# Optimization experiments

Measured on AMD Instinct MI355X. Metric: run time of the kernel, lower is better.

The kernel has to match this reference:

```python
import jax, jax.numpy as jnp
import numpy as np

# static config matching init_kwargs
NODE, K, KER, STR = 32, 10, 5, 2
B, C = 8, 64
N = NODE * NODE          # 1024 nodes per sample
BN = B * N               # 8192 total nodes
OUT = (NODE - KER) // STR + 1
E = OUT * OUT            # local hyperedges per sample (196)
BN_EPS = 1e-5


def _local_block_diag():
    """Static block-diagonal local incidence matrix (BN, B*E), built once in numpy."""
    idx = np.arange(N).reshape(NODE, NODE)
    H_local = np.zeros((N, E), np.float32)
    e = 0
    for i in range(0, NODE - KER + 1, STR):
        for j in range(0, NODE - KER + 1, STR):
            H_local[idx[i:i + KER, j:j + KER].ravel(), e] = 1.0
            e += 1
    blk = np.zeros((BN, B * E), np.float32)
    for b in range(B):
        blk[b * N:(b + 1) * N, b * E:(b + 1) * E] = H_local
    return jnp.asarray(blk)


_LOCAL_BLK = _local_block_diag()


def setup_inputs() -> dict:
    key = jax.random.key(0)
    k1, k2 = jax.random.split(key, 2)
    x = jax.random.normal(k1, (B, N, C), jnp.float32)
    W_conv = jax.random.normal(k2, (C, C), jnp.float32) * 0.05
    b_conv = jnp.zeros((C,), jnp.float32)
    gamma = jnp.ones((C,), jnp.float32)
    beta = jnp.zeros((C,), jnp.float32)
    return {"x": x, "W_conv": W_conv, "b_conv": b_conv, "gamma": gamma, "beta": beta}


def reference(x, W_conv, b_conv, gamma, beta):
    xm = x.reshape(BN, C)                       # merged nodes (B*N, C)

    # --- hypergraph construction (no_grad in torch) ---
    xs = jax.lax.stop_gradient(xm)
    sq = jnp.sum(xs * xs, axis=-1, keepdims=True)
    dists = sq - 2.0 * (xs @ xs.T) + sq.T       # (BN, BN) pairwise sq-dists
    _, inds = jax.lax.top_k(-dists, K + 1)      # K+1 smallest distances
    # weights_function(prob=False) -> all ones; scatter incidence
    H = jnp.zeros((BN, BN), x.dtype).at[jnp.arange(BN)[:, None], inds].set(1.0)
    # Dv == K+1 for every row -> max_k = K+1 and the second topk gives new_H == H
    Hfull = jnp.concatenate([H, _LOCAL_BLK], axis=1)  # (BN, BN + B*E)

    # G = Dv^{-1/2} H W De^{-1} H^T Dv^{-1/2}, W = I, via diagonal scaling
    DV = Hfull.sum(axis=1)
    DE = jnp.maximum(Hfull.sum(axis=0), 1e-8)
    dv2 = DV ** -0.5
    A = dv2[:, None] * Hfull
    G = (A * (1.0 / DE)[None, :]) @ A.T          # (BN, BN)
    G = jax.lax.stop_gradient(G)

    # --- HGNN conv: linear -> G matmul -> BN (train stats) -> relu -> residual ---
    y = xm @ W_conv.T + b_conv                   # (BN, C)
    z = G @ y                                    # (BN, C)
    mu = z.mean(axis=0)
    var = z.var(axis=0)                          # biased, as torch BN training
    zn = (z - mu) / jnp.sqrt(var + BN_EPS) * gamma + beta
    out = jax.nn.relu(zn) + xm
    return out.reshape(B, N, C)
```

## Files before the change

kernel.cpp:

```cpp
#include <hip/hip_runtime.h>
#include <math.h>

#define BNTOT 8192
#define CH    64
#define KP1   11
#define NLOC  1568
#define MARGIN 1.0f
#define LCAPR 256

typedef __attribute__((ext_vector_type(8))) short short8;
typedef __attribute__((ext_vector_type(4))) float float4v;

__device__ __forceinline__ int pcnt(int p) {
  int lo = p - 4; if (lo < 0) lo = 0; lo += (lo & 1);
  int hi = p; if (hi > 26) hi = 26;
  return (hi >= lo) ? (((hi - lo) >> 1) + 1) : 0;
}
__device__ __forceinline__ float dv2_of(int u) {
  int node = u & 1023;
  int rr = node >> 5, cc = node & 31;
  int dv = KP1 + pcnt(rr) * pcnt(cc);
  return 1.0f / sqrtf((float)dv);
}
__device__ __forceinline__ unsigned short f2bf(float f) {
  unsigned u = __float_as_uint(f);
  unsigned r = (u + 0x7FFFu + ((u >> 16) & 1u)) >> 16;
  return (unsigned short)r;
}
__device__ __forceinline__ unsigned fkey(float s) {
  unsigned u = __float_as_uint(s);
  return (u & 0x80000000u) ? ~u : (u | 0x80000000u);
}
__device__ __forceinline__ unsigned long long skey(float s, int idx) {
  return ((unsigned long long)fkey(s) << 32) | (unsigned)idx;
}
__device__ __forceinline__ int mbcnt64(unsigned long long m) {
  return __builtin_amdgcn_mbcnt_hi((unsigned)(m >> 32),
         __builtin_amdgcn_mbcnt_lo((unsigned)m, 0));
}

__global__ void k_cast(const float* __restrict__ X, unsigned short* __restrict__ Xh,
                       float* __restrict__ sq) {
  int g = blockIdx.x * 256 + threadIdx.x;
  int lane = threadIdx.x & 63;
  float v = X[g];
  Xh[g] = f2bf(v);
  float s = v * v;
  #pragma unroll
  for (int off = 32; off >= 1; off >>= 1) s += __shfl_xor(s, off, 64);
  if (lane == 0) sq[g >> 6] = s;
}

__global__ __launch_bounds__(256)
void k_thrpart(const float* __restrict__ X, const float* __restrict__ sq,
               float* __restrict__ part) {
  const int tid = threadIdx.x, wave = tid >> 6, lane = tid & 63;
  const int rg = blockIdx.x >> 3, chunk = blockIdx.x & 7;
  const int row = rg * 64 + lane;
  float xr[CH];
  {
    const float4* xp = (const float4*)(X + (size_t)row * CH);
    #pragma unroll
    for (int k = 0; k < CH / 4; ++k) {
      float4 v = xp[k];
      xr[4*k+0] = v.x; xr[4*k+1] = v.y; xr[4*k+2] = v.z; xr[4*k+3] = v.w;
    }
  }
  float tv[KP1];
  #pragma unroll
  for (int t = 0; t < KP1; ++t) tv[t] = INFINITY;

  for (int s = 0; s < 32; ++s) {
    int j = __builtin_amdgcn_readfirstlane(((chunk * 4 + wave) * 32 + s) * 8);
    const float* cp = X + (size_t)j * CH;
    float d0 = 0.f, d1 = 0.f, d2 = 0.f, d3 = 0.f;
    #pragma unroll
    for (int k = 0; k < CH / 4; ++k) {
      d0 = fmaf(xr[4*k+0], cp[4*k+0], d0);
      d1 = fmaf(xr[4*k+1], cp[4*k+1], d1);
      d2 = fmaf(xr[4*k+2], cp[4*k+2], d2);
      d3 = fmaf(xr[4*k+3], cp[4*k+3], d3);
    }
    float cv = fmaf(-2.0f, (d0 + d1) + (d2 + d3), sq[j]);
    #pragma unroll
    for (int t = 0; t < KP1; ++t) {
      float lo = fminf(tv[t], cv), hi = fmaxf(tv[t], cv);
      tv[t] = lo; cv = hi;
    }
  }
  __shared__ float ls[4][64][KP1];
  #pragma unroll
  for (int t = 0; t < KP1; ++t) ls[wave][lane][t] = tv[t];
  __syncthreads();
  if (tid < 64) {
    float v[KP1];
    #pragma unroll
    for (int t = 0; t < KP1; ++t) v[t] = ls[0][tid][t];
    #pragma unroll
    for (int w = 1; w < 4; ++w)
      #pragma unroll
      for (int t = 0; t < KP1; ++t) {
        float cv = ls[w][tid][t];
        #pragma unroll
        for (int s2 = 0; s2 < KP1; ++s2) {
          float lo = fminf(v[s2], cv), hi = fmaxf(v[s2], cv);
          v[s2] = lo; cv = hi;
        }
      }
    size_t base = ((size_t)blockIdx.x * 64 + tid) * KP1;
    #pragma unroll
    for (int t = 0; t < KP1; ++t) part[base + t] = v[t];
  }
}

__global__ void k_thrmerge(const float* __restrict__ part, float* __restrict__ thr) {
  const int rg = blockIdx.x, lane = threadIdx.x;
  const int row = rg * 64 + lane;
  float v[KP1];
  {
    size_t b0 = ((size_t)(rg * 8) * 64 + lane) * KP1;
    #pragma unroll
    for (int t = 0; t < KP1; ++t) v[t] = part[b0 + t];
  }
  for (int c = 1; c < 8; ++c) {
    size_t b = ((size_t)(rg * 8 + c) * 64 + lane) * KP1;
    #pragma unroll
    for (int t = 0; t < KP1; ++t) {
      float cv = part[b + t];
      #pragma unroll
      for (int s2 = 0; s2 < KP1; ++s2) {
        float lo = fminf(v[s2], cv), hi = fmaxf(v[s2], cv);
        v[s2] = lo; cv = hi;
      }
    }
  }
  thr[row] = v[KP1 - 1] + MARGIN;
}

__global__ __launch_bounds__(256)
void k_filter(const unsigned short* __restrict__ Xh, const float* __restrict__ sq,
              const float* __restrict__ thr, unsigned long long* __restrict__ mask) {
  const int tid = threadIdx.x, wave = tid >> 6, lane = tid & 63;
  const int m = lane & 15, q = lane >> 4;
  const int rowbase = (blockIdx.x >> 5) * 64;
  const int colbase = (blockIdx.x & 31) * 256 + wave * 64;
  const int wcol = (blockIdx.x & 31) * 4 + wave;

  short8 a[4][2];
  #pragma unroll
  for (int rt = 0; rt < 4; ++rt)
    #pragma unroll
    for (int kc = 0; kc < 2; ++kc)
      a[rt][kc] = *(const short8*)(Xh + (size_t)(rowbase + rt * 16 + m) * CH + kc * 32 + q * 8);

  short8 b0[4], b1[4];
  float sqv[4];
  #pragma unroll
  for (int sub = 0; sub < 4; ++sub) {
    const int coln = colbase + sub * 16 + m;
    const short8* bp = (const short8*)(Xh + (size_t)coln * CH + q * 8);
    b0[sub] = bp[0];
    b1[sub] = bp[4];
    sqv[sub] = sq[coln];
  }

  float thrv[16];
  #pragma unroll
  for (int rt = 0; rt < 4; ++rt)
    #pragma unroll
    for (int r = 0; r < 4; ++r)
      thrv[rt * 4 + r] = thr[rowbase + rt * 16 + q * 4 + r];

  const float4v cz = {0.f, 0.f, 0.f, 0.f};
  const int sr = lane & 15, qq = sr >> 2, rr = sr & 3;

  #pragma unroll
  for (int rt = 0; rt < 4; ++rt) {
    unsigned long long bal[4][4];
    #pragma unroll
    for (int sub = 0; sub < 4; ++sub) {
      float4v c = __builtin_amdgcn_mfma_f32_16x16x32_bf16(a[rt][0], b0[sub], cz, 0, 0, 0);
      c = __builtin_amdgcn_mfma_f32_16x16x32_bf16(a[rt][1], b1[sub], c, 0, 0, 0);
      #pragma unroll
      for (int r = 0; r < 4; ++r) {
        float score = fmaf(-2.0f, c[r], sqv[sub]);
        bal[sub][r] = __ballot(score < thrv[rt * 4 + r]);
      }
    }
    unsigned long long w = 0;
    #pragma unroll
    for (int sub = 0; sub < 4; ++sub) {
      unsigned long long bsel = (rr == 0) ? bal[sub][0]
                              : (rr == 1) ? bal[sub][1]
                              : (rr == 2) ? bal[sub][2]
                              :             bal[sub][3];
      unsigned long long slice = (bsel >> (qq * 16)) & 0xFFFFull;
      w |= slice << (sub * 16);
    }
    if ((lane >> 4) == rt)
      mask[(size_t)(rowbase + rt * 16 + sr) * 128 + wcol] = w;
  }
}

__global__ __launch_bounds__(256)
void k_rescore(const float* __restrict__ X, const float* __restrict__ sq,
               const unsigned long long* __restrict__ mask,
               int* __restrict__ inds, int* __restrict__ DE) {
  __shared__ int cols[4][LCAPR];
  const int tid = threadIdx.x, lane = tid & 63, wv = tid >> 6;
  const int row = __builtin_amdgcn_readfirstlane(blockIdx.x * 4 + wv);

  float xr[CH];
  {
    const float4* xp = (const float4*)(X + (size_t)row * CH);
    #pragma unroll
    for (int k = 0; k < CH / 4; ++k) {
      float4 v = xp[k];
      xr[4*k+0] = v.x; xr[4*k+1] = v.y; xr[4*k+2] = v.z; xr[4*k+3] = v.w;
    }
  }

  const unsigned long long* mrow = mask + (size_t)row * 128;
  unsigned long long w0 = mrow[lane * 2 + 0];
  unsigned long long w1 = mrow[lane * 2 + 1];

  int cnt = __popcll(w0) + __popcll(w1);
  int p = 0, total = 0;
  #pragma unroll
  for (int b = 0; b < 8; ++b) {
    unsigned long long bb = __ballot((cnt >> b) & 1);
    p     += mbcnt64(bb) << b;
    total += __popcll(bb) << b;
  }

  if (total <= LCAPR) {
    unsigned long long w = w0;
    while (w) { int b = __builtin_ctzll(w); w &= w - 1; cols[wv][p++] = lane * 128 + b; }
    w = w1;
    while (w) { int b = __builtin_ctzll(w); w &= w - 1; cols[wv][p++] = lane * 128 + 64 + b; }

    unsigned kscore[4]; int kidx[4];
    #pragma unroll
    for (int a = 0; a < 4; ++a) { kscore[a] = 0xFFFFFFFFu; kidx[a] = 0; }
    const int slots = (total + 63) >> 6;
    for (int a = 0; a < slots; ++a) {
      int s = a * 64 + lane;
      if (s < total) {
        int cj = cols[wv][s];
        const float4* cp = (const float4*)(X + (size_t)cj * CH);
        float d0 = 0.f, d1 = 0.f, d2 = 0.f, d3 = 0.f;
        #pragma unroll
        for (int k = 0; k < CH / 4; ++k) {
          float4 v = cp[k];
          d0 = fmaf(xr[4*k+0], v.x, d0);
          d1 = fmaf(xr[4*k+1], v.y, d1);
          d2 = fmaf(xr[4*k+2], v.z, d2);
          d3 = fmaf(xr[4*k+3], v.w, d3);
        }
        float score = fmaf(-2.0f, (d0 + d1) + (d2 + d3), sq[cj]);
        kscore[a] = fkey(score);
        kidx[a] = cj;
      }
    }

    unsigned long long blo = 0, bhi = 1ull << 32;
    #pragma unroll 4
    for (int it = 0; it < 32; ++it) {
      unsigned mid = (unsigned)((blo + bhi) >> 1);
      int l = (kscore[0] < mid) + (kscore[1] < mid) + (kscore[2] < mid) + (kscore[3] < mid);
      int c = __popcll(__ballot(l & 1)) + 2 * __popcll(__ballot(l & 2))
            + 4 * __popcll(__ballot(l & 4));
      if (c < KP1) blo = mid; else bhi = mid;
    }
    const unsigned T = (unsigned)blo;

    int ll = (kscore[0] < T) + (kscore[1] < T) + (kscore[2] < T) + (kscore[3] < T);
    int c_less = __popcll(__ballot(ll & 1)) + 2 * __popcll(__ballot(ll & 2))
               + 4 * __popcll(__ballot(ll & 4));
    int le = (kscore[0] <= T) + (kscore[1] <= T) + (kscore[2] <= T) + (kscore[3] <= T);
    int c_le = __popcll(__ballot(le & 1)) + 2 * __popcll(__ballot(le & 2))
             + 4 * __popcll(__ballot(le & 4));
    const int needed = KP1 - c_less;
    const int cnt_eq = c_le - c_less;

    unsigned idxcut = BNTOT;
    if (cnt_eq != needed) {
      int lo2 = 0, hi2 = BNTOT;
      for (int it = 0; it < 13; ++it) {
        int mid2 = (lo2 + hi2) >> 1;
        int l2 = ((kscore[0] == T) & (kidx[0] < mid2)) + ((kscore[1] == T) & (kidx[1] < mid2))
               + ((kscore[2] == T) & (kidx[2] < mid2)) + ((kscore[3] == T) & (kidx[3] < mid2));
        int c2 = __popcll(__ballot(l2 & 1)) + 2 * __popcll(__ballot(l2 & 2))
               + 4 * __popcll(__ballot(l2 & 4));
        if (c2 < needed) lo2 = mid2; else hi2 = mid2;
      }
      idxcut = (unsigned)hi2;
    }

    int base = 0;
    #pragma unroll
    for (int a = 0; a < 4; ++a) {
      bool win = (kscore[a] < T) | ((kscore[a] == T) & ((unsigned)kidx[a] < idxcut));
      unsigned long long bal = __ballot(win);
      int pos = base + mbcnt64(bal);
      if (win) {
        inds[(size_t)row * KP1 + pos] = kidx[a];
        atomicAdd(&DE[kidx[a]], 1);
      }
      base += __popcll(bal);
    }
  } else {
    float tv[KP1]; int ti[KP1];
    #pragma unroll
    for (int t = 0; t < KP1; ++t) { tv[t] = INFINITY; ti[t] = -1; }
    for (int s = lane; s < BNTOT; s += 64) {
      const float4* cp = (const float4*)(X + (size_t)s * CH);
      float d0 = 0.f, d1 = 0.f, d2 = 0.f, d3 = 0.f;
      #pragma unroll
      for (int k = 0; k < CH / 4; ++k) {
        float4 v = cp[k];
        d0 = fmaf(xr[4*k+0], v.x, d0);
        d1 = fmaf(xr[4*k+1], v.y, d1);
        d2 = fmaf(xr[4*k+2], v.z, d2);
        d3 = fmaf(xr[4*k+3], v.w, d3);
      }
      float score = fmaf(-2.0f, (d0 + d1) + (d2 + d3), sq[s]);
      if (score < tv[KP1 - 1]) {
        float cv = score; int ci = s;
        #pragma unroll
        for (int t = 0; t < KP1; ++t) {
          bool sw = cv < tv[t];
          float nv = sw ? cv    : tv[t]; int ni = sw ? ti[t] : ti[t];
          ni = sw ? ci : ti[t];
          float ov = sw ? tv[t] : cv;    int oi = sw ? ti[t] : ci;
          tv[t] = nv; ti[t] = ni; cv = ov; ci = oi;
        }
      }
    }
    unsigned long long cur = skey(tv[0], ti[0]);
    unsigned long long keep = 0;
    #pragma unroll
    for (int t = 0; t < KP1; ++t) {
      unsigned long long mw = cur;
      #pragma unroll
      for (int off = 1; off < 64; off <<= 1) {
        unsigned lo = __shfl_xor((unsigned)mw, off, 64);
        unsigned hi = __shfl_xor((unsigned)(mw >> 32), off, 64);
        unsigned long long o = ((unsigned long long)hi << 32) | lo;
        mw = (o < mw) ? o : mw;
      }
      if (lane == t) keep = mw;
      if (cur == mw) {
        #pragma unroll
        for (int q = 0; q < KP1 - 1; ++q) { tv[q] = tv[q+1]; ti[q] = ti[q+1]; }
        tv[KP1-1] = INFINITY; ti[KP1-1] = -1;
        cur = skey(tv[0], ti[0]);
      }
    }
    if (lane < KP1) {
      int idx = (int)(unsigned)(keep & 0xFFFFFFFFull);
      inds[(size_t)row * KP1 + lane] = idx;
      atomicAdd(&DE[idx], 1);
    }
  }
}

__global__ void k_lin(const float* __restrict__ X, const float* __restrict__ W,
                      const float* __restrict__ bias, float* __restrict__ t) {
  int lane = threadIdx.x & 63;
  int wave = threadIdx.x >> 6;
  int rowbase = (blockIdx.x * 4 + wave) * 4;
  float wr[CH];
  {
    const float4* wp = (const float4*)(W + (size_t)lane * CH);
    #pragma unroll
    for (int k = 0; k < CH / 4; ++k) {
      float4 v = wp[k];
      wr[4*k+0] = v.x; wr[4*k+1] = v.y; wr[4*k+2] = v.z; wr[4*k+3] = v.w;
    }
  }
  float bc = bias[lane];
  #pragma unroll
  for (int r = 0; r < 4; ++r) {
    int row = __builtin_amdgcn_readfirstlane(rowbase + r);
    const float* xp = X + (size_t)row * CH;
    float d0 = 0.f, d1 = 0.f, d2 = 0.f, d3 = 0.f;
    #pragma unroll
    for (int k = 0; k < CH / 4; ++k) {
      d0 = fmaf(wr[4*k+0], xp[4*k+0], d0);
      d1 = fmaf(wr[4*k+1], xp[4*k+1], d1);
      d2 = fmaf(wr[4*k+2], xp[4*k+2], d2);
      d3 = fmaf(wr[4*k+3], xp[4*k+3], d3);
    }
    float y = (d0 + d1) + (d2 + d3) + bc;
    t[(size_t)row * CH + lane] = y * dv2_of(row);
  }
}

__global__ void k_edge(const float* __restrict__ t, const int* __restrict__ inds,
                       float* __restrict__ s_knn, float* __restrict__ s_loc) {
  int c = threadIdx.x & 63;
  int w = threadIdx.x >> 6;
  if (blockIdx.x < BNTOT / 4) {
    int u = blockIdx.x * 4 + w;
    float val = t[(size_t)u * CH + c];
    int ub = __builtin_amdgcn_readfirstlane(u);
    const int* ip = inds + (size_t)ub * KP1;
    #pragma unroll
    for (int j = 0; j < KP1; ++j) {
      int e = ip[j];
      atomicAdd(&s_knn[(size_t)e * CH + c], val);
    }
  } else {
    int e = (blockIdx.x - BNTOT / 4) * 4 + w;
    int b  = e / 196;
    int le = e - b * 196;
    int pi = le / 14;
    int pj = le - pi * 14;
    int base = b * 1024 + (pi * 2) * 32 + pj * 2;
    float acc = 0.f;
    #pragma unroll
    for (int di = 0; di < 5; ++di)
      #pragma unroll
      for (int dj = 0; dj < 5; ++dj)
        acc += t[(size_t)(base + di * 32 + dj) * CH + c];
    s_loc[(size_t)e * CH + c] = acc * (1.0f / 25.0f);
  }
}

__global__ void k_gatherbn(const float* __restrict__ s_knn, const float* __restrict__ s_loc,
                           const int* __restrict__ inds, const int* __restrict__ DE,
                           float* __restrict__ z, float* __restrict__ part,
                           float* __restrict__ partsq) {
  int c = threadIdx.x & 63;
  int w = threadIdx.x >> 6;
  int u = blockIdx.x * 4 + w;
  int ub = __builtin_amdgcn_readfirstlane(u);
  const int* ip = inds + (size_t)ub * KP1;
  float acc = 0.f;
  #pragma unroll
  for (int j = 0; j < KP1; ++j) {
    int e = ip[j];
    float invde = 1.0f / (float)DE[e];
    acc += s_knn[(size_t)e * CH + c] * invde;
  }
  int node = ub & 1023, b = ub >> 10;
  int rr = node >> 5, cc = node & 31;
  int i0 = rr - 4; if (i0 < 0) i0 = 0; i0 += (i0 & 1);
  int i1 = rr; if (i1 > 26) i1 = 26;
  int j0 = cc - 4; if (j0 < 0) j0 = 0; j0 += (j0 & 1);
  int j1 = cc; if (j1 > 26) j1 = 26;
  for (int i = i0; i <= i1; i += 2)
    for (int jj = j0; jj <= j1; jj += 2) {
      int e = b * 196 + (i >> 1) * 14 + (jj >> 1);
      acc += s_loc[(size_t)e * CH + c];
    }
  float zv = acc * dv2_of(ub);
  z[(size_t)ub * CH + c] = zv;

  __shared__ float ls[4][CH], ls2[4][CH];
  ls[w][c] = zv; ls2[w][c] = zv * zv;
  __syncthreads();
  if (threadIdx.x < 64) {
    part[(size_t)blockIdx.x * CH + c]   = ls[0][c] + ls[1][c] + ls[2][c] + ls[3][c];
    partsq[(size_t)blockIdx.x * CH + c] = ls2[0][c] + ls2[1][c] + ls2[2][c] + ls2[3][c];
  }
}

__global__ void k_bnfin1(const float* __restrict__ part, const float* __restrict__ partsq,
                         float* __restrict__ part2, float* __restrict__ partsq2) {
  int c = threadIdx.x & 63;
  int rq = threadIdx.x >> 6;
  int blk = blockIdx.x;
  float s = 0.f, s2 = 0.f;
  for (int k = 0; k < 16; ++k) {
    size_t r = (size_t)(blk * 64 + rq * 16 + k) * CH + c;
    s += part[r]; s2 += partsq[r];
  }
  __shared__ float ls[4][CH], ls2[4][CH];
  ls[rq][c] = s; ls2[rq][c] = s2;
  __syncthreads();
  if (rq == 0) {
    part2[(size_t)blk * CH + c]   = ls[0][c] + ls[1][c] + ls[2][c] + ls[3][c];
    partsq2[(size_t)blk * CH + c] = ls2[0][c] + ls2[1][c] + ls2[2][c] + ls2[3][c];
  }
}

__global__ void k_out(const float* __restrict__ z, const float* __restrict__ X,
                      const float* __restrict__ part2, const float* __restrict__ partsq2,
                      const float* __restrict__ gamma, const float* __restrict__ beta,
                      float* __restrict__ out) {
  __shared__ float ls[4][CH], ls2[4][CH], smu[CH], srstd[CH];
  int c = threadIdx.x & 63;
  int w = threadIdx.x >> 6;
  float s = 0.f, s2 = 0.f;
  #pragma unroll
  for (int b = 0; b < 8; ++b) {
    size_t r = (size_t)(w * 8 + b) * CH + c;
    s += part2[r]; s2 += partsq2[r];
  }
  ls[w][c] = s; ls2[w][c] = s2;
  __syncthreads();
  if (threadIdx.x < 64) {
    float S  = ls[0][c] + ls[1][c] + ls[2][c] + ls[3][c];
    float S2 = ls2[0][c] + ls2[1][c] + ls2[2][c] + ls2[3][c];
    float m = S * (1.0f / (float)BNTOT);
    float var = S2 * (1.0f / (float)BNTOT) - m * m;
    smu[c] = m;
    srstd[c] = 1.0f / sqrtf(var + 1e-5f);
  }
  __syncthreads();

  int u = blockIdx.x * 4 + w;
  size_t idx = (size_t)u * CH + c;
  float zn = (z[idx] - smu[c]) * srstd[c] * gamma[c] + beta[c];
  out[idx] = fmaxf(zn, 0.f) + X[idx];
}

extern "C" void kernel_launch(void* const* d_in, const int* in_sizes, int n_in,
                              void* d_out, int out_size, void* d_ws, size_t ws_size,
                              hipStream_t stream) {
  const float* X     = (const float*)d_in[0];
  const float* W     = (const float*)d_in[1];
  const float* bias  = (const float*)d_in[2];
  const float* gamma = (const float*)d_in[3];
  const float* beta  = (const float*)d_in[4];
  float* out = (float*)d_out;

  float* ws = (float*)d_ws;
  float* sq      = ws;
  float* thr     = sq + 8192;
  float* t       = thr + 8192;
  float* s_loc   = t + 524288;
  float* z       = s_loc + 100352;
  float* part    = z + 524288;
  float* partsq  = part + 131072;
  float* part2   = partsq + 131072;
  float* partsq2 = part2 + 2048;
  float* thrpart = partsq2 + 2048;
  int*   inds    = (int*)(thrpart + 720896);
  unsigned short* Xh = (unsigned short*)(inds + 90112);
  unsigned long long* mask = (unsigned long long*)(Xh + 524288);
  int*   DE     = (int*)(mask + (size_t)8192 * 128);
  float* s_knn  = (float*)(DE + 8192);

  hipMemsetAsync(DE, 0, (size_t)(8192 + 524288) * 4, stream);

  k_cast    <<<2048, 256, 0, stream>>>(X, Xh, sq);
  k_thrpart <<<1024, 256, 0, stream>>>(X, sq, thrpart);
  k_thrmerge<<<128, 64, 0, stream>>>(thrpart, thr);
  k_filter  <<<4096, 256, 0, stream>>>(Xh, sq, thr, mask);
  k_rescore <<<2048, 256, 0, stream>>>(X, sq, mask, inds, DE);
  k_lin     <<<512, 256, 0, stream>>>(X, W, bias, t);
  k_edge    <<<BNTOT / 4 + NLOC / 4, 256, 0, stream>>>(t, inds, s_knn, s_loc);
  k_gatherbn<<<BNTOT / 4, 256, 0, stream>>>(s_knn, s_loc, inds, DE, z, part, partsq);
  k_bnfin1  <<<32, 256, 0, stream>>>(part, partsq, part2, partsq2);
  k_out     <<<BNTOT / 4, 256, 0, stream>>>(z, X, part2, partsq2, gamma, beta, out);

  (void)in_sizes; (void)n_in; (void)out_size; (void)ws_size;
}
```

Before: 232.9 us.

## Widen rescore candidate cap and fold BN stats into binned atomics

Raises the per-row candidate cap in the rescore kernel from 256 to 512 and fully unrolls the scoring into 8 register slots, so fewer rows fall back to the slow brute-force 8192-column scan. It also removes the k_bnfin1 reduction kernel: gatherbn now atomically accumulates per-channel sums into 8 bins, and k_out reduces those bins directly. The trade is more registers and more unconditional loads per wave in rescore, plus float-atomic nondeterminism in the BN statistics.

```diff
diff --git a/kernel.cpp b/kernel.cpp
--- a/kernel.cpp
+++ b/kernel.cpp
@@ -6,7 +6,7 @@
 #define KP1   11
 #define NLOC  1568
 #define MARGIN 1.0f
-#define LCAPR 256
+#define LCAPR 512
 
 typedef __attribute__((ext_vector_type(8))) short short8;
 typedef __attribute__((ext_vector_type(4))) float float4v;
@@ -37,6 +37,12 @@
 __device__ __forceinline__ int mbcnt64(unsigned long long m) {
   return __builtin_amdgcn_mbcnt_hi((unsigned)(m >> 32),
          __builtin_amdgcn_mbcnt_lo((unsigned)m, 0));
+}
+__device__ __forceinline__ int wave_count4(int l) {
+  return     __popcll(__ballot(l & 1))
+       + 2 * __popcll(__ballot(l & 2))
+       + 4 * __popcll(__ballot(l & 4))
+       + 8 * __popcll(__ballot(l & 8));
 }
 
 __global__ void k_cast(const float* __restrict__ X, unsigned short* __restrict__ Xh,
@@ -239,47 +245,43 @@
     w = w1;
     while (w) { int b = __builtin_ctzll(w); w &= w - 1; cols[wv][p++] = lane * 128 + 64 + b; }
 
-    unsigned kscore[4]; int kidx[4];
-    #pragma unroll
-    for (int a = 0; a < 4; ++a) { kscore[a] = 0xFFFFFFFFu; kidx[a] = 0; }
-    const int slots = (total + 63) >> 6;
-    for (int a = 0; a < slots; ++a) {
+    unsigned kscore[8]; int kidx[8];
+    #pragma unroll
+    for (int a = 0; a < 8; ++a) { kscore[a] = 0xFFFFFFFFu; kidx[a] = 0; }
+    #pragma unroll
+    for (int a = 0; a < 8; ++a) {
       int s = a * 64 + lane;
-      if (s < total) {
-        int cj = cols[wv][s];
-        const float4* cp = (const float4*)(X + (size_t)cj * CH);
-        float d0 = 0.f, d1 = 0.f, d2 = 0.f, d3 = 0.f;
-        #pragma unroll
-        for (int k = 0; k < CH / 4; ++k) {
-          float4 v = cp[k];
-          d0 = fmaf(xr[4*k+0], v.x, d0);
-          d1 = fmaf(xr[4*k+1], v.y, d1);
-          d2 = fmaf(xr[4*k+2], v.z, d2);
-          d3 = fmaf(xr[4*k+3], v.w, d3);
-        }
-        float score = fmaf(-2.0f, (d0 + d1) + (d2 + d3), sq[cj]);
-        kscore[a] = fkey(score);
-        kidx[a] = cj;
-      }
+      bool valid = s < total;
+      int cj = cols[wv][valid ? s : 0];
+      const float4* cp = (const float4*)(X + (size_t)cj * CH);
+      float d0 = 0.f, d1 = 0.f, d2 = 0.f, d3 = 0.f;
+      #pragma unroll
+      for (int k = 0; k < CH / 4; ++k) {
+        float4 v = cp[k];
+        d0 = fmaf(xr[4*k+0], v.x, d0);
+        d1 = fmaf(xr[4*k+1], v.y, d1);
+        d2 = fmaf(xr[4*k+2], v.z, d2);
+        d3 = fmaf(xr[4*k+3], v.w, d3);
+      }
+      float score = fmaf(-2.0f, (d0 + d1) + (d2 + d3), sq[cj]);
+      if (valid) { kscore[a] = fkey(score); kidx[a] = cj; }
     }
 
     unsigned long long blo = 0, bhi = 1ull << 32;
-    #pragma unroll 4
     for (int it = 0; it < 32; ++it) {
       unsigned mid = (unsigned)((blo + bhi) >> 1);
-      int l = (kscore[0] < mid) + (kscore[1] < mid) + (kscore[2] < mid) + (kscore[3] < mid);
-      int c = __popcll(__ballot(l & 1)) + 2 * __popcll(__ballot(l & 2))
-            + 4 * __popcll(__ballot(l & 4));
-      if (c < KP1) blo = mid; else bhi = mid;
+      int l = 0;
+      #pragma unroll
+      for (int a = 0; a < 8; ++a) l += (kscore[a] < mid);
+      if (wave_count4(l) < KP1) blo = mid; else bhi = mid;
     }
     const unsigned T = (unsigned)blo;
 
-    int ll = (kscore[0] < T) + (kscore[1] < T) + (kscore[2] < T) + (kscore[3] < T);
-    int c_less = __popcll(__ballot(ll & 1)) + 2 * __popcll(__ballot(ll & 2))
-               + 4 * __popcll(__ballot(ll & 4));
-    int le = (kscore[0] <= T) + (kscore[1] <= T) + (kscore[2] <= T) + (kscore[3] <= T);
-    int c_le = __popcll(__ballot(le & 1)) + 2 * __popcll(__ballot(le & 2))
-             + 4 * __popcll(__ballot(le & 4));
+    int ll = 0, le = 0;
+    #pragma unroll
+    for (int a = 0; a < 8; ++a) { ll += (kscore[a] < T); le += (kscore[a] <= T); }
+    int c_less = wave_count4(ll);
+    int c_le   = wave_count4(le);
     const int needed = KP1 - c_less;
     const int cnt_eq = c_le - c_less;
 
@@ -288,18 +290,17 @@
       int lo2 = 0, hi2 = BNTOT;
       for (int it = 0; it < 13; ++it) {
         int mid2 = (lo2 + hi2) >> 1;
-        int l2 = ((kscore[0] == T) & (kidx[0] < mid2)) + ((kscore[1] == T) & (kidx[1] < mid2))
-               + ((kscore[2] == T) & (kidx[2] < mid2)) + ((kscore[3] == T) & (kidx[3] < mid2));
-        int c2 = __popcll(__ballot(l2 & 1)) + 2 * __popcll(__ballot(l2 & 2))
-               + 4 * __popcll(__ballot(l2 & 4));
-        if (c2 < needed) lo2 = mid2; else hi2 = mid2;
+        int l2 = 0;
+        #pragma unroll
+        for (int a = 0; a < 8; ++a) l2 += ((kscore[a] == T) & (kidx[a] < mid2));
+        if (wave_count4(l2) < needed) lo2 = mid2; else hi2 = mid2;
       }
       idxcut = (unsigned)hi2;
     }
 
     int base = 0;
     #pragma unroll
-    for (int a = 0; a < 4; ++a) {
+    for (int a = 0; a < 8; ++a) {
       bool win = (kscore[a] < T) | ((kscore[a] == T) & ((unsigned)kidx[a] < idxcut));
       unsigned long long bal = __ballot(win);
       int pos = base + mbcnt64(bal);
@@ -330,8 +331,7 @@
         #pragma unroll
         for (int t = 0; t < KP1; ++t) {
           bool sw = cv < tv[t];
-          float nv = sw ? cv    : tv[t]; int ni = sw ? ti[t] : ti[t];
-          ni = sw ? ci : ti[t];
+          float nv = sw ? cv    : tv[t]; int ni = sw ? ci    : ti[t];
           float ov = sw ? tv[t] : cv;    int oi = sw ? ti[t] : ci;
           tv[t] = nv; ti[t] = ni; cv = ov; ci = oi;
         }
@@ -430,8 +430,8 @@
 
 __global__ void k_gatherbn(const float* __restrict__ s_knn, const float* __restrict__ s_loc,
                            const int* __restrict__ inds, const int* __restrict__ DE,
-                           float* __restrict__ z, float* __restrict__ part,
-                           float* __restrict__ partsq) {
+                           float* __restrict__ z, float* __restrict__ gsum,
+                           float* __restrict__ gsumsq) {
   int c = threadIdx.x & 63;
   int w = threadIdx.x >> 6;
   int u = blockIdx.x * 4 + w;
@@ -462,58 +462,31 @@
   ls[w][c] = zv; ls2[w][c] = zv * zv;
   __syncthreads();
   if (threadIdx.x < 64) {
-    part[(size_t)blockIdx.x * CH + c]   = ls[0][c] + ls[1][c] + ls[2][c] + ls[3][c];
-    partsq[(size_t)blockIdx.x * CH + c] = ls2[0][c] + ls2[1][c] + ls2[2][c] + ls2[3][c];
-  }
-}
-
-__global__ void k_bnfin1(const float* __restrict__ part, const float* __restrict__ partsq,
-                         float* __restrict__ part2, float* __restrict__ partsq2) {
-  int c = threadIdx.x & 63;
-  int rq = threadIdx.x >> 6;
-  int blk = blockIdx.x;
-  float s = 0.f, s2 = 0.f;
-  for (int k = 0; k < 16; ++k) {
-    size_t r = (size_t)(blk * 64 + rq * 16 + k) * CH + c;
-    s += part[r]; s2 += partsq[r];
-  }
-  __shared__ float ls[4][CH], ls2[4][CH];
-  ls[rq][c] = s; ls2[rq][c] = s2;
-  __syncthreads();
-  if (rq == 0) {
-    part2[(size_t)blk * CH + c]   = ls[0][c] + ls[1][c] + ls[2][c] + ls[3][c];
-    partsq2[(size_t)blk * CH + c] = ls2[0][c] + ls2[1][c] + ls2[2][c] + ls2[3][c];
+    int bin = (blockIdx.x & 7) * CH;
+    atomicAdd(&gsum[bin + c],   ls[0][c] + ls[1][c] + ls[2][c] + ls[3][c]);
+    atomicAdd(&gsumsq[bin + c], ls2[0][c] + ls2[1][c] + ls2[2][c] + ls2[3][c]);
   }
 }
 
 __global__ void k_out(const float* __restrict__ z, const float* __restrict__ X,
-                      const float* __restrict__ part2, const float* __restrict__ partsq2,
+                      const float* __restrict__ gsum, const float* __restrict__ gsumsq,
                       const float* __restrict__ gamma, const float* __restrict__ beta,
                       float* __restrict__ out) {
-  __shared__ float ls[4][CH], ls2[4][CH], smu[CH], srstd[CH];
   int c = threadIdx.x & 63;
   int w = threadIdx.x >> 6;
-  float s = 0.f, s2 = 0.f;
+  float S = 0.f, S2 = 0.f;
   #pragma unroll
   for (int b = 0; b < 8; ++b) {
-    size_t r = (size_t)(w * 8 + b) * CH + c;
-    s += part2[r]; s2 += partsq2[r];
-  }
-  ls[w][c] = s; ls2[w][c] = s2;
-  __syncthreads();
-  if (threadIdx.x < 64) {
-    float S  = ls[0][c] + ls[1][c] + ls[2][c] + ls[3][c];
-    float S2 = ls2[0][c] + ls2[1][c] + ls2[2][c] + ls2[3][c];
-    float m = S * (1.0f / (float)BNTOT);
-    float var = S2 * (1.0f / (float)BNTOT) - m * m;
-    smu[c] = m;
-    srstd[c] = 1.0f / sqrtf(var + 1e-5f);
-  }
-  __syncthreads();
+    S  += gsum[b * CH + c];
+    S2 += gsumsq[b * CH + c];
+  }
+  float m = S * (1.0f / (float)BNTOT);
+  float var = S2 * (1.0f / (float)BNTOT) - m * m;
+  float rstd = 1.0f / sqrtf(var + 1e-5f);
 
   int u = blockIdx.x * 4 + w;
   size_t idx = (size_t)u * CH + c;
-  float zn = (z[idx] - smu[c]) * srstd[c] * gamma[c] + beta[c];
+  float zn = (z[idx] - m) * rstd * gamma[c] + beta[c];
   out[idx] = fmaxf(zn, 0.f) + X[idx];
 }
 
@@ -533,18 +506,16 @@
   float* t       = thr + 8192;
   float* s_loc   = t + 524288;
   float* z       = s_loc + 100352;
-  float* part    = z + 524288;
-  float* partsq  = part + 131072;
-  float* part2   = partsq + 131072;
-  float* partsq2 = part2 + 2048;
-  float* thrpart = partsq2 + 2048;
+  float* thrpart = z + 524288;
   int*   inds    = (int*)(thrpart + 720896);
   unsigned short* Xh = (unsigned short*)(inds + 90112);
   unsigned long long* mask = (unsigned long long*)(Xh + 524288);
   int*   DE     = (int*)(mask + (size_t)8192 * 128);
-  float* s_knn  = (float*)(DE + 8192);
-
-  hipMemsetAsync(DE, 0, (size_t)(8192 + 524288) * 4, stream);
+  float* gsum   = (float*)(DE + 8192);
+  float* gsumsq = gsum + 512;
+  float* s_knn  = gsumsq + 512;
+
+  hipMemsetAsync(DE, 0, (size_t)(8192 + 512 + 512 + 524288) * 4, stream);
 
   k_cast    <<<2048, 256, 0, stream>>>(X, Xh, sq);
   k_thrpart <<<1024, 256, 0, stream>>>(X, sq, thrpart);
@@ -553,9 +524,8 @@
   k_rescore <<<2048, 256, 0, stream>>>(X, sq, mask, inds, DE);
   k_lin     <<<512, 256, 0, stream>>>(X, W, bias, t);
   k_edge    <<<BNTOT / 4 + NLOC / 4, 256, 0, stream>>>(t, inds, s_knn, s_loc);
-  k_gatherbn<<<BNTOT / 4, 256, 0, stream>>>(s_knn, s_loc, inds, DE, z, part, partsq);
-  k_bnfin1  <<<32, 256, 0, stream>>>(part, partsq, part2, partsq2);
-  k_out     <<<BNTOT / 4, 256, 0, stream>>>(z, X, part2, partsq2, gamma, beta, out);
+  k_gatherbn<<<BNTOT / 4, 256, 0, stream>>>(s_knn, s_loc, inds, DE, z, gsum, gsumsq);
+  k_out     <<<BNTOT / 4, 256, 0, stream>>>(z, X, gsum, gsumsq, gamma, beta, out);
 
   (void)in_sizes; (void)n_in; (void)out_size; (void)ws_size;
 }
```

Result: slower. 240.5 us (+3.3%).
